# Kernel tuning notes

Hardware: AMD Instinct MI355X
Metric: run time of the kernel (lower is better)

## Reference

```python
import jax, jax.numpy as jnp
import numpy as np

N_QUBITS = 16
N_LAYERS = 6
BATCH = 512


def _apply_1q(state, U, q, n, batched):
    """Apply a single-qubit gate U to qubit q of state (B, 2**n).
    U: (2,2) shared, or (B,2,2) per-sample if batched."""
    B = state.shape[0]
    d0, d1 = 2 ** q, 2 ** (n - q - 1)
    s = state.reshape(B, d0, 2, d1)
    if batched:
        s = jnp.einsum('bij,bxjy->bxiy', U, s)
    else:
        s = jnp.einsum('ij,bxjy->bxiy', U, s)
    return s.reshape(B, -1)


def _apply_cnot(state, c, t, n):
    """CNOT with control c, target t on state (B, 2**n)."""
    B = state.shape[0]
    a, b = (c, t) if c < t else (t, c)
    d0, d1, d2 = 2 ** a, 2 ** (b - a - 1), 2 ** (n - b - 1)
    s = state.reshape(B, d0, 2, d1, 2, d2)
    if c < t:  # control = axis 2, target = axis 4: flip target where control==1
        s = jnp.concatenate([s[:, :, :1], jnp.flip(s[:, :, 1:], axis=4)], axis=2)
    else:      # control = axis 4, target = axis 2
        s = jnp.concatenate([s[:, :, :, :, :1], jnp.flip(s[:, :, :, :, 1:], axis=2)], axis=4)
    return s.reshape(B, -1)


def _rx(theta):
    """RX(theta) for a batch of angles -> (B,2,2) complex64."""
    c = jnp.cos(theta * 0.5).astype(jnp.complex64)
    s = (-1j * jnp.sin(theta * 0.5)).astype(jnp.complex64)
    return jnp.stack([jnp.stack([c, s], -1), jnp.stack([s, c], -1)], -2)


def _rot(phi, theta, omega):
    """PennyLane Rot(phi,theta,omega) = RZ(omega) RY(theta) RZ(phi) -> (2,2) complex64."""
    c = jnp.cos(theta * 0.5)
    s = jnp.sin(theta * 0.5)
    m00 = jnp.exp(-0.5j * (phi + omega)) * c
    m01 = -jnp.exp(0.5j * (phi - omega)) * s
    m10 = jnp.exp(-0.5j * (phi - omega)) * s
    m11 = jnp.exp(0.5j * (phi + omega)) * c
    return jnp.stack([jnp.stack([m00, m01]), jnp.stack([m10, m11])]).astype(jnp.complex64)


def _circuit(x, weights, n, n_layers):
    B = x.shape[0]
    state = jnp.zeros((B, 2 ** n), dtype=jnp.complex64).at[:, 0].set(1.0)
    # AngleEmbedding: default rotation is RX(x_q) on wire q (per-sample angles)
    for q in range(n):
        state = _apply_1q(state, _rx(x[:, q]), q, n, batched=True)
    # StronglyEntanglingLayers: Rot on each wire, then ring of CNOTs with range r
    for l in range(n_layers):
        for q in range(n):
            U = _rot(weights[l, q, 0], weights[l, q, 1], weights[l, q, 2])
            state = _apply_1q(state, U, q, n, batched=False)
        r = (l % (n - 1)) + 1  # PennyLane default ranges
        for q in range(n):
            state = _apply_cnot(state, q, (q + r) % n, n)
    # <Z_q> = P(bit_q = 0) - P(bit_q = 1)
    probs = state.real ** 2 + state.imag ** 2  # (B, 2**n)
    exps = []
    for q in range(n):
        p = probs.reshape(B, 2 ** q, 2, -1).sum(axis=(1, 3))  # (B, 2)
        exps.append(p[:, 0] - p[:, 1])
    return jnp.stack(exps, axis=-1)  # (B, n)


def setup_inputs() -> dict:
    key = jax.random.key(0)
    kx, kw = jax.random.split(key)
    x = jax.random.normal(kx, (BATCH, N_QUBITS), dtype=jnp.float32)
    weights = jax.random.normal(kw, (N_LAYERS, N_QUBITS, 3), dtype=jnp.float32)
    return {"x": x, "weights": weights}


def reference(x, weights):
    return _circuit(x, weights, N_QUBITS, N_LAYERS)
```

## Files before the change

kernel.cpp:

```cpp
#include <hip/hip_runtime.h>


#define NTH 512
typedef float v16f __attribute__((ext_vector_type(16)));

template <int I> struct IC { static constexpr int value = I; };
template <int N, int I = 0, typename F>
__device__ __forceinline__ void static_for(F&& f) {
  if constexpr (I < N) { f(IC<I>{}); static_for<N, I + 1>(f); }
}

template <int SH, int E> struct EIdx { static constexpr int v = (E & 1) | ((E >> 1) << SH); };


template <int LB>
__device__ __forceinline__ void rot_local(v16f& ar, v16f& ai, const float* __restrict__ u) {
  const float u00r = u[0], u00i = u[1], u01r = u[2], u01i = u[3];
  const float u10r = u[4], u10i = u[5], u11r = u[6], u11i = u[7];
  static_for<8>([&](auto hc) {
    constexpr int h = hc.value;
    constexpr int e0 = ((h >> LB) << (LB + 1)) | (h & ((1 << LB) - 1));
    constexpr int e1 = e0 | (1 << LB);
    const float axr = ar[e0], axi = ai[e0], bxr = ar[e1], bxi = ai[e1];
    ar[e0] = u00r * axr - u00i * axi + u01r * bxr - u01i * bxi;
    ai[e0] = u00r * axi + u00i * axr + u01r * bxi + u01i * bxr;
    ar[e1] = u10r * axr - u10i * axi + u11r * bxr - u11i * bxi;
    ai[e1] = u10r * axi + u10i * axr + u11r * bxi + u11i * bxr;
  });
}

__device__ __forceinline__ void rot_lane(v16f& ar, v16f& ai, const float* __restrict__ u,
                                         const int m, const int bit) {
  const float car = bit ? u[6] : u[0], cai = bit ? u[7] : u[1];
  const float cbr = bit ? u[4] : u[2], cbi = bit ? u[5] : u[3];
  static_for<16>([&](auto ec) {
    constexpr int e = ec.value;
    const float orr = ar[e], oii = ai[e];
    const float pr = __shfl_xor(orr, m);
    const float pi = __shfl_xor(oii, m);
    ar[e] = car * orr - cai * oii + cbr * pr - cbi * pi;
    ai[e] = car * oii + cai * orr + cbr * pi + cbi * pr;
  });
}

template <int SH, int C>
__device__ __forceinline__ void cnot_lane(v16f& ar, v16f& ai, const int m, const int ibase) {
  if constexpr ((EIdx<SH, 15>::v >> C) & 1) {
    static_for<16>([&](auto ec) {
      constexpr int e = ec.value;
      if constexpr ((EIdx<SH, e>::v >> C) & 1) {
        ar[e] = __shfl_xor(ar[e], m);
        ai[e] = __shfl_xor(ai[e], m);
      }
    });
  } else {
    if ((ibase >> C) & 1) {
      static_for<16>([&](auto ec) {
        constexpr int e = ec.value;
        ar[e] = __shfl_xor(ar[e], m);
        ai[e] = __shfl_xor(ai[e], m);
      });
    }
  }
}

template <int TB, int SH, int C>
__device__ __forceinline__ void cnot_local(v16f& ar, v16f& ai, const int ibase) {
  static_for<8>([&](auto hc) {
    constexpr int h = hc.value;
    constexpr int e0 = ((h >> TB) << (TB + 1)) | (h & ((1 << TB) - 1));
    constexpr int e1 = e0 | (1 << TB);
    if constexpr ((EIdx<SH, 15>::v >> C) & 1) {
      if constexpr ((EIdx<SH, e0>::v >> C) & 1) {
        const float tr = ar[e0], ti = ai[e0];
        ar[e0] = ar[e1]; ai[e0] = ai[e1];
        ar[e1] = tr;     ai[e1] = ti;
      }
    } else {
      const int take = (ibase >> C) & 1;
      const float axr = ar[e0], axi = ai[e0], bxr = ar[e1], bxi = ai[e1];
      ar[e0] = take ? bxr : axr; ai[e0] = take ? bxi : axi;
      ar[e1] = take ? axr : bxr; ai[e1] = take ? axi : bxi;
    }
  });
}

__global__ void qsim_prep(const float* __restrict__ w, float* __restrict__ gm) {
  const int i = threadIdx.x;
  if (i < 96) {
    const float phi = w[i * 3 + 0];
    const float th  = w[i * 3 + 1];
    const float om  = w[i * 3 + 2];
    float st, ct; sincosf(0.5f * th, &st, &ct);
    float sa, ca; sincosf(0.5f * (phi + om), &sa, &ca);
    float sb, cb; sincosf(0.5f * (phi - om), &sb, &cb);
    float* u = gm + i * 8;
    u[0] =  ct * ca; u[1] = -ct * sa;
    u[2] = -st * cb; u[3] = -st * sb;
    u[4] =  st * cb; u[5] = -st * sb;
    u[6] =  ct * ca; u[7] =  ct * sa;
  }
}

template <int L>
__global__ void __launch_bounds__(NTH) sweepP(float2* __restrict__ st,
                                              const float* __restrict__ x,
                                              const float* __restrict__ gm) {
  const int tid = threadIdx.x;
  const int s  = blockIdx.x >> 3;
  const int fb = blockIdx.x & 7;
  const int ibase = ((tid & 7) << 4) | (((tid >> 3) & 7) << 7) |
                    (((tid >> 6) & 7) << 10) | (fb << 13);
  const int pbase = ((tid & 7) << 1) | (((tid >> 6) & 7) << 7) | (fb << 10) |
                    (((tid >> 3) & 7) << 13);
  float2* __restrict__ base = st + (s << 16) + pbase;
  constexpr int r = L + 1;
  const float* __restrict__ gl = gm + L * 128;
  v16f ar, ai;

  if constexpr (L == 0) {
    __shared__ float iv[16][4];
    if (tid < 16) {
      const float* u = gm + tid * 8;
      float sx, cx; sincosf(0.5f * x[s * 16 + tid], &sx, &cx);
      iv[tid][0] = u[0] * cx + u[3] * sx;
      iv[tid][1] = u[1] * cx - u[2] * sx;
      iv[tid][2] = u[4] * cx + u[7] * sx;
      iv[tid][3] = u[5] * cx - u[6] * sx;
    }
    __syncthreads();
    float Tr = 1.f, Ti = 0.f;
    #pragma unroll
    for (int b = 4; b <= 15; ++b) {
      const int bit = (ibase >> b) & 1;
      const float fr = iv[b][2 * bit], fi = iv[b][2 * bit + 1];
      const float nr = Tr * fr - Ti * fi; Ti = Tr * fi + Ti * fr; Tr = nr;
    }
    ar[0] = Tr; ai[0] = Ti;
    static_for<4>([&](auto bc) {
      constexpr int bI = bc.value;
      const float v0r = iv[bI][0], v0i = iv[bI][1], v1r = iv[bI][2], v1i = iv[bI][3];
      static_for<(1 << bI)>([&](auto kc) {
        constexpr int k = kc.value;
        constexpr int k1 = k | (1 << bI);
        const float kr = ar[k], ki = ai[k];
        ar[k1] = kr * v1r - ki * v1i; ai[k1] = kr * v1i + ki * v1r;
        ar[k]  = kr * v0r - ki * v0i; ai[k]  = kr * v0i + ki * v0r;
      });
    });
  } else {
    #pragma unroll
    for (int eh = 0; eh < 8; ++eh) {
      const float4 v = *reinterpret_cast<const float4*>(base + (eh << 4));
      ar[2 * eh] = v.x; ai[2 * eh] = v.y; ar[2 * eh + 1] = v.z; ai[2 * eh + 1] = v.w;
    }
    static_for<L>([&](auto kc) {
      constexpr int k = kc.value;
      constexpr int C = 16 - L + k;
      if constexpr (k <= 3) cnot_local<k, 1, C>(ar, ai, ibase);
      else                  cnot_lane<1, C>(ar, ai, 1 << (k - 4), ibase);
    });
    rot_local<0>(ar, ai, gl);
    rot_local<1>(ar, ai, gl + 8);
    rot_local<2>(ar, ai, gl + 16);
    rot_local<3>(ar, ai, gl + 24);
    #pragma unroll
    for (int q = 4; q <= 9; ++q)
      rot_lane(ar, ai, gl + q * 8, 1 << (q - 4), (tid >> (q - 4)) & 1);
  }

  static_for<10 - r>([&](auto gc) {
    constexpr int g = gc.value;
    constexpr int t = g + r;
    if constexpr (t <= 3) cnot_local<t, 1, g>(ar, ai, ibase);
    else                  cnot_lane<1, g>(ar, ai, 1 << (t - 4), ibase);
  });

  #pragma unroll
  for (int eh = 0; eh < 8; ++eh)
    *reinterpret_cast<float4*>(base + (eh << 4)) =
        make_float4(ar[2 * eh], ai[2 * eh], ar[2 * eh + 1], ai[2 * eh + 1]);
}

template <int L>
__global__ void __launch_bounds__(NTH) sweepQ(float2* __restrict__ st,
                                              const float* __restrict__ gm) {
  const int tid = threadIdx.x;
  const int s  = blockIdx.x >> 3;
  const int fb = blockIdx.x & 7;
  const int ibase = ((tid & 7) << 4) | (((tid >> 3) & 7) << 13) |
                    (((tid >> 6) & 7) << 7) | (fb << 1);
  const int pbase = ((tid & 7) << 1) | (((tid >> 3) & 7) << 10) |
                    (((tid >> 6) & 7) << 13) | (fb << 4);
  float2* __restrict__ base = st + (s << 16) + pbase;
  constexpr int r = L + 1;
  const float* __restrict__ gl = gm + L * 128;
  v16f ar, ai;
  #pragma unroll
  for (int eh = 0; eh < 8; ++eh) {
    const float4 v = *reinterpret_cast<const float4*>(base + (eh << 7));
    ar[2 * eh] = v.x; ai[2 * eh] = v.y; ar[2 * eh + 1] = v.z; ai[2 * eh + 1] = v.w;
  }
  if constexpr (L > 0) {
    rot_local<1>(ar, ai, gl + 80);
    rot_local<2>(ar, ai, gl + 88);
    rot_local<3>(ar, ai, gl + 96);
    rot_lane(ar, ai, gl + 104, 8,  (tid >> 3) & 1);
    rot_lane(ar, ai, gl + 112, 16, (tid >> 4) & 1);
    rot_lane(ar, ai, gl + 120, 32, (tid >> 5) & 1);
  }
  static_for<6>([&](auto gc) {
    constexpr int g = 10 - r + gc.value;
    constexpr int t = g + r;
    if constexpr (t >= 13) cnot_lane<10, g>(ar, ai, 1 << (t - 10), ibase);
    else                   cnot_local<t - 9, 10, g>(ar, ai, ibase);
  });

  #pragma unroll
  for (int eh = 0; eh < 8; ++eh)
    *reinterpret_cast<float4*>(base + (eh << 7)) =
        make_float4(ar[2 * eh], ai[2 * eh], ar[2 * eh + 1], ai[2 * eh + 1]);
}

__global__ void __launch_bounds__(NTH) finalK(const float2* __restrict__ st,
                                              float* __restrict__ part) {
  const int tid = threadIdx.x;
  const int s  = blockIdx.x >> 3;
  const int fb = blockIdx.x & 7;
  const int ibase = ((tid & 7) << 4) | (((tid >> 3) & 7) << 7) |
                    (((tid >> 6) & 7) << 10) | (fb << 13);
  const int pbase = ((tid & 7) << 1) | (((tid >> 6) & 7) << 7) | (fb << 10) |
                    (((tid >> 3) & 7) << 13);
  const float2* __restrict__ base = st + (s << 16) + pbase;
  v16f ar, ai;
  #pragma unroll
  for (int eh = 0; eh < 8; ++eh) {
    const float4 v = *reinterpret_cast<const float4*>(base + (eh << 4));
    ar[2 * eh] = v.x; ai[2 * eh] = v.y; ar[2 * eh + 1] = v.z; ai[2 * eh + 1] = v.w;
  }
  static_for<6>([&](auto kc) {
    constexpr int k = kc.value;
    constexpr int C = 10 + k;
    if constexpr (k <= 3) cnot_local<k, 1, C>(ar, ai, ibase);
    else                  cnot_lane<1, C>(ar, ai, 1 << (k - 4), ibase);
  });
  __shared__ float red[8][16];
  float tot = 0.f, sl0 = 0.f, sl1 = 0.f, sl2 = 0.f, sl3 = 0.f;
  static_for<16>([&](auto ec) {
    constexpr int e = ec.value;
    const float p = ar[e] * ar[e] + ai[e] * ai[e];
    tot += p;
    if constexpr (e & 1) sl0 -= p; else sl0 += p;
    if constexpr (e & 2) sl1 -= p; else sl1 += p;
    if constexpr (e & 4) sl2 -= p; else sl2 += p;
    if constexpr (e & 8) sl3 -= p; else sl3 += p;
  });
  const float sl[4] = {sl0, sl1, sl2, sl3};
  const int wv = tid >> 6;
  static_for<16>([&](auto qc) {
    constexpr int q = qc.value;
    float v;
    if constexpr (q < 4) v = sl[q];
    else v = ((ibase >> q) & 1) ? -tot : tot;
    v += __shfl_xor(v, 1);  v += __shfl_xor(v, 2);  v += __shfl_xor(v, 4);
    v += __shfl_xor(v, 8);  v += __shfl_xor(v, 16); v += __shfl_xor(v, 32);
    if ((tid & 63) == 0) red[wv][q] = v;
  });
  __syncthreads();
  if (tid < 16) {
    float a = 0.f;
    #pragma unroll
    for (int w8 = 0; w8 < 8; ++w8) a += red[w8][tid];
    part[blockIdx.x * 16 + tid] = a;
  }
}

__global__ void __launch_bounds__(NTH) reduceK(const float* __restrict__ part,
                                               float* __restrict__ out) {
  const int j = blockIdx.x * NTH + threadIdx.x;
  const int s = j >> 4, q = j & 15;
  float a = 0.f;
  #pragma unroll
  for (int fb = 0; fb < 8; ++fb) a += part[(s << 7) + fb * 16 + q];
  out[j] = a;
}

extern "C" void kernel_launch(void* const* d_in, const int* in_sizes, int n_in,
                              void* d_out, int out_size, void* d_ws, size_t ws_size,
                              hipStream_t stream) {
  (void)in_sizes; (void)n_in; (void)out_size;
  const float* x = (const float*)d_in[0];
  const float* w = (const float*)d_in[1];
  float* out = (float*)d_out;
  float* gm   = (float*)d_ws;
  float* part = (float*)((char*)d_ws + 4096);
  float2* st  = (float2*)((char*)d_ws + 524288);

  const size_t avail = ws_size > 524288 ? ws_size - 524288 : 0;
  long long chunk = (long long)(avail / 524288);
  if (chunk > 256) chunk = 256;
  if (chunk < 1) chunk = 1;

  qsim_prep<<<dim3(1), dim3(128), 0, stream>>>(w, gm);
  for (int s0 = 0; s0 < 512; s0 += (int)chunk) {
    const int ns = (512 - s0) < (int)chunk ? (512 - s0) : (int)chunk;
    const dim3 g(ns * 8), b(NTH);
    const float* xs = x + s0 * 16;
    float* pp = part + (size_t)s0 * 128;
    sweepP<0><<<g, b, 0, stream>>>(st, xs, gm);
    sweepQ<0><<<g, b, 0, stream>>>(st, gm);
    sweepP<1><<<g, b, 0, stream>>>(st, xs, gm);
    sweepQ<1><<<g, b, 0, stream>>>(st, gm);
    sweepP<2><<<g, b, 0, stream>>>(st, xs, gm);
    sweepQ<2><<<g, b, 0, stream>>>(st, gm);
    sweepP<3><<<g, b, 0, stream>>>(st, xs, gm);
    sweepQ<3><<<g, b, 0, stream>>>(st, gm);
    sweepP<4><<<g, b, 0, stream>>>(st, xs, gm);
    sweepQ<4><<<g, b, 0, stream>>>(st, gm);
    sweepP<5><<<g, b, 0, stream>>>(st, xs, gm);
    sweepQ<5><<<g, b, 0, stream>>>(st, gm);
    finalK<<<g, b, 0, stream>>>(st, pp);
  }
  reduceK<<<dim3(16), dim3(NTH), 0, stream>>>(part, out);
}
```

Measured before the change: 1.579 ms.

## Move some rot_lane gates into the preceding kernel and use nontemporal stores

Some single-qubit rotations on lane-distributed qubits of the next layer are moved from the first sweep kernel into the end of the second sweep kernel, for the qubits whose CNOT dependencies allow it. This rebalances the per-kernel work and cuts the number of cross-lane shuffle gates in the first kernel. Global stores and the final load are switched to nontemporal builtins to reduce cache pollution on the streaming state. The risk is that reordering gates across kernels breaks correctness if the commutation assumptions are wrong, and nontemporal hints may bypass caches that were helping the reloads.

```diff
diff --git a/kernel.cpp b/kernel.cpp
--- a/kernel.cpp
+++ b/kernel.cpp
@@ -3,11 +3,20 @@
 
 #define NTH 512
 typedef float v16f __attribute__((ext_vector_type(16)));
+typedef float f4 __attribute__((ext_vector_type(4)));
 
 template <int I> struct IC { static constexpr int value = I; };
 template <int N, int I = 0, typename F>
 __device__ __forceinline__ void static_for(F&& f) {
   if constexpr (I < N) { f(IC<I>{}); static_for<N, I + 1>(f); }
+}
+
+__device__ __forceinline__ void nt_store4(float2* p, float a, float b, float c, float d) {
+  f4 v; v.x = a; v.y = b; v.z = c; v.w = d;
+  __builtin_nontemporal_store(v, reinterpret_cast<f4*>(p));
+}
+__device__ __forceinline__ f4 nt_load4(const float2* p) {
+  return __builtin_nontemporal_load(reinterpret_cast<const f4*>(p));
 }
 
 template <int SH, int E> struct EIdx { static constexpr int v = (E & 1) | ((E >> 1) << SH); };
@@ -164,9 +173,10 @@
     rot_local<1>(ar, ai, gl + 8);
     rot_local<2>(ar, ai, gl + 16);
     rot_local<3>(ar, ai, gl + 24);
-    #pragma unroll
-    for (int q = 4; q <= 9; ++q)
-      rot_lane(ar, ai, gl + q * 8, 1 << (q - 4), (tid >> (q - 4)) & 1);
+    if constexpr (L == 5) rot_lane(ar, ai, gl + 32, 1, tid & 1);
+    rot_lane(ar, ai, gl + 56, 8,  (tid >> 3) & 1);
+    rot_lane(ar, ai, gl + 64, 16, (tid >> 4) & 1);
+    rot_lane(ar, ai, gl + 72, 32, (tid >> 5) & 1);
   }
 
   static_for<10 - r>([&](auto gc) {
@@ -178,8 +188,7 @@
 
   #pragma unroll
   for (int eh = 0; eh < 8; ++eh)
-    *reinterpret_cast<float4*>(base + (eh << 4)) =
-        make_float4(ar[2 * eh], ai[2 * eh], ar[2 * eh + 1], ai[2 * eh + 1]);
+    nt_store4(base + (eh << 4), ar[2 * eh], ai[2 * eh], ar[2 * eh + 1], ai[2 * eh + 1]);
 }
 
 template <int L>
@@ -215,11 +224,21 @@
     if constexpr (t >= 13) cnot_lane<10, g>(ar, ai, 1 << (t - 10), ibase);
     else                   cnot_local<t - 9, 10, g>(ar, ai, ibase);
   });
+  if constexpr (L <= 3) {
+    const float* __restrict__ gn = gm + (L + 1) * 128;
+    rot_lane(ar, ai, gn + 32, 1, tid & 1);
+    rot_lane(ar, ai, gn + 40, 2, (tid >> 1) & 1);
+    rot_lane(ar, ai, gn + 48, 4, (tid >> 2) & 1);
+  }
+  if constexpr (L == 4) {
+    const float* __restrict__ gn = gm + 5 * 128;
+    rot_lane(ar, ai, gn + 40, 2, (tid >> 1) & 1);
+    rot_lane(ar, ai, gn + 48, 4, (tid >> 2) & 1);
+  }
 
   #pragma unroll
   for (int eh = 0; eh < 8; ++eh)
-    *reinterpret_cast<float4*>(base + (eh << 7)) =
-        make_float4(ar[2 * eh], ai[2 * eh], ar[2 * eh + 1], ai[2 * eh + 1]);
+    nt_store4(base + (eh << 7), ar[2 * eh], ai[2 * eh], ar[2 * eh + 1], ai[2 * eh + 1]);
 }
 
 __global__ void __launch_bounds__(NTH) finalK(const float2* __restrict__ st,
@@ -235,7 +254,7 @@
   v16f ar, ai;
   #pragma unroll
   for (int eh = 0; eh < 8; ++eh) {
-    const float4 v = *reinterpret_cast<const float4*>(base + (eh << 4));
+    const f4 v = nt_load4(base + (eh << 4));
     ar[2 * eh] = v.x; ai[2 * eh] = v.y; ar[2 * eh + 1] = v.z; ai[2 * eh + 1] = v.w;
   }
   static_for<6>([&](auto kc) {
```

Result: no change. 1.596 ms (+1.1%).

## Hold 32 amplitudes per thread and remap qubit bits across sweep kernels

Applied to the files above, without the earlier changes.

Doubles the per-thread register tile from 16 to 32 complex amplitudes, so each thread keeps 5 qubits local and blocks cover a quarter of a sample instead of an eighth. The qubit-to-register/lane/block bit mappings in sweepP, sweepQ and finalK are reworked so more gates and CNOTs run in registers and fewer need lane shuffles. The cnot and rot helpers are generalised to the new layout. The intent is less shuffle and grid overhead per gate, at the cost of higher register pressure and, in sweepQ, narrower strided float2 accesses instead of float4 loads.

```diff
diff --git a/kernel.cpp b/kernel.cpp
--- a/kernel.cpp
+++ b/kernel.cpp
@@ -2,7 +2,7 @@
 
 
 #define NTH 512
-typedef float v16f __attribute__((ext_vector_type(16)));
+typedef float v32f __attribute__((ext_vector_type(32)));
 
 template <int I> struct IC { static constexpr int value = I; };
 template <int N, int I = 0, typename F>
@@ -10,14 +10,12 @@
   if constexpr (I < N) { f(IC<I>{}); static_for<N, I + 1>(f); }
 }
 
-template <int SH, int E> struct EIdx { static constexpr int v = (E & 1) | ((E >> 1) << SH); };
-
 
 template <int LB>
-__device__ __forceinline__ void rot_local(v16f& ar, v16f& ai, const float* __restrict__ u) {
+__device__ __forceinline__ void rot_local(v32f& ar, v32f& ai, const float* __restrict__ u) {
   const float u00r = u[0], u00i = u[1], u01r = u[2], u01i = u[3];
   const float u10r = u[4], u10i = u[5], u11r = u[6], u11i = u[7];
-  static_for<8>([&](auto hc) {
+  static_for<16>([&](auto hc) {
     constexpr int h = hc.value;
     constexpr int e0 = ((h >> LB) << (LB + 1)) | (h & ((1 << LB) - 1));
     constexpr int e1 = e0 | (1 << LB);
@@ -29,11 +27,11 @@
   });
 }
 
-__device__ __forceinline__ void rot_lane(v16f& ar, v16f& ai, const float* __restrict__ u,
+__device__ __forceinline__ void rot_lane(v32f& ar, v32f& ai, const float* __restrict__ u,
                                          const int m, const int bit) {
   const float car = bit ? u[6] : u[0], cai = bit ? u[7] : u[1];
   const float cbr = bit ? u[4] : u[2], cbi = bit ? u[5] : u[3];
-  static_for<16>([&](auto ec) {
+  static_for<32>([&](auto ec) {
     constexpr int e = ec.value;
     const float orr = ar[e], oii = ai[e];
     const float pr = __shfl_xor(orr, m);
@@ -43,35 +41,14 @@
   });
 }
 
-template <int SH, int C>
-__device__ __forceinline__ void cnot_lane(v16f& ar, v16f& ai, const int m, const int ibase) {
-  if constexpr ((EIdx<SH, 15>::v >> C) & 1) {
-    static_for<16>([&](auto ec) {
-      constexpr int e = ec.value;
-      if constexpr ((EIdx<SH, e>::v >> C) & 1) {
-        ar[e] = __shfl_xor(ar[e], m);
-        ai[e] = __shfl_xor(ai[e], m);
-      }
-    });
-  } else {
-    if ((ibase >> C) & 1) {
-      static_for<16>([&](auto ec) {
-        constexpr int e = ec.value;
-        ar[e] = __shfl_xor(ar[e], m);
-        ai[e] = __shfl_xor(ai[e], m);
-      });
-    }
-  }
-}
-
-template <int TB, int SH, int C>
-__device__ __forceinline__ void cnot_local(v16f& ar, v16f& ai, const int ibase) {
-  static_for<8>([&](auto hc) {
+template <int TB, int LOCALLO, int C>
+__device__ __forceinline__ void cnot_local(v32f& ar, v32f& ai, const int ibase) {
+  static_for<16>([&](auto hc) {
     constexpr int h = hc.value;
     constexpr int e0 = ((h >> TB) << (TB + 1)) | (h & ((1 << TB) - 1));
     constexpr int e1 = e0 | (1 << TB);
-    if constexpr ((EIdx<SH, 15>::v >> C) & 1) {
-      if constexpr ((EIdx<SH, e0>::v >> C) & 1) {
+    if constexpr (C >= LOCALLO && C < LOCALLO + 5) {
+      if constexpr ((e0 >> (C - LOCALLO)) & 1) {
         const float tr = ar[e0], ti = ai[e0];
         ar[e0] = ar[e1]; ai[e0] = ai[e1];
         ar[e1] = tr;     ai[e1] = ti;
@@ -83,6 +60,28 @@
       ar[e1] = take ? axr : bxr; ai[e1] = take ? axi : bxi;
     }
   });
+}
+
+template <int LOCALLO, int C>
+__device__ __forceinline__ void cnot_lane(v32f& ar, v32f& ai, const int m, const int ibase) {
+  if constexpr (C >= LOCALLO && C < LOCALLO + 5) {
+    static_for<32>([&](auto ec) {
+      constexpr int e = ec.value;
+      if constexpr ((e >> (C - LOCALLO)) & 1) {
+        ar[e] = __shfl_xor(ar[e], m);
+        ai[e] = __shfl_xor(ai[e], m);
+      }
+    });
+  } else {
+    const int take = (ibase >> C) & 1;
+    static_for<32>([&](auto ec) {
+      constexpr int e = ec.value;
+      const float pr = __shfl_xor(ar[e], m);
+      const float pi = __shfl_xor(ai[e], m);
+      ar[e] = take ? pr : ar[e];
+      ai[e] = take ? pi : ai[e];
+    });
+  }
 }
 
 __global__ void qsim_prep(const float* __restrict__ w, float* __restrict__ gm) {
@@ -107,16 +106,16 @@
                                               const float* __restrict__ x,
                                               const float* __restrict__ gm) {
   const int tid = threadIdx.x;
-  const int s  = blockIdx.x >> 3;
-  const int fb = blockIdx.x & 7;
-  const int ibase = ((tid & 7) << 4) | (((tid >> 3) & 7) << 7) |
-                    (((tid >> 6) & 7) << 10) | (fb << 13);
-  const int pbase = ((tid & 7) << 1) | (((tid >> 6) & 7) << 7) | (fb << 10) |
-                    (((tid >> 3) & 7) << 13);
+  const int s  = blockIdx.x >> 2;
+  const int fb = blockIdx.x & 3;
+  const int ibase = (((tid >> 3) & 7) << 5) | (((tid >> 6) & 7) << 8) |
+                    (fb << 11) | ((tid & 7) << 13);
+  const int pbase = (((tid >> 3) & 7) << 1) | ((tid & 7) << 4) |
+                    (((tid >> 6) & 7) << 11) | (fb << 14);
   float2* __restrict__ base = st + (s << 16) + pbase;
   constexpr int r = L + 1;
   const float* __restrict__ gl = gm + L * 128;
-  v16f ar, ai;
+  v32f ar, ai;
 
   if constexpr (L == 0) {
     __shared__ float iv[16][4];
@@ -131,13 +130,13 @@
     __syncthreads();
     float Tr = 1.f, Ti = 0.f;
     #pragma unroll
-    for (int b = 4; b <= 15; ++b) {
+    for (int b = 5; b <= 15; ++b) {
       const int bit = (ibase >> b) & 1;
       const float fr = iv[b][2 * bit], fi = iv[b][2 * bit + 1];
       const float nr = Tr * fr - Ti * fi; Ti = Tr * fi + Ti * fr; Tr = nr;
     }
     ar[0] = Tr; ai[0] = Ti;
-    static_for<4>([&](auto bc) {
+    static_for<5>([&](auto bc) {
       constexpr int bI = bc.value;
       const float v0r = iv[bI][0], v0i = iv[bI][1], v1r = iv[bI][2], v1i = iv[bI][3];
       static_for<(1 << bI)>([&](auto kc) {
@@ -150,35 +149,36 @@
     });
   } else {
     #pragma unroll
-    for (int eh = 0; eh < 8; ++eh) {
-      const float4 v = *reinterpret_cast<const float4*>(base + (eh << 4));
+    for (int eh = 0; eh < 16; ++eh) {
+      const float4 v = *reinterpret_cast<const float4*>(base + (eh << 7));
       ar[2 * eh] = v.x; ai[2 * eh] = v.y; ar[2 * eh + 1] = v.z; ai[2 * eh + 1] = v.w;
     }
     static_for<L>([&](auto kc) {
       constexpr int k = kc.value;
       constexpr int C = 16 - L + k;
-      if constexpr (k <= 3) cnot_local<k, 1, C>(ar, ai, ibase);
-      else                  cnot_lane<1, C>(ar, ai, 1 << (k - 4), ibase);
+      if constexpr (k <= 4) cnot_local<k, 0, C>(ar, ai, ibase);
+      else                  cnot_lane<0, C>(ar, ai, 8, ibase);
     });
     rot_local<0>(ar, ai, gl);
     rot_local<1>(ar, ai, gl + 8);
     rot_local<2>(ar, ai, gl + 16);
     rot_local<3>(ar, ai, gl + 24);
-    #pragma unroll
-    for (int q = 4; q <= 9; ++q)
-      rot_lane(ar, ai, gl + q * 8, 1 << (q - 4), (tid >> (q - 4)) & 1);
-  }
-
-  static_for<10 - r>([&](auto gc) {
+    rot_local<4>(ar, ai, gl + 32);
+    rot_lane(ar, ai, gl + 40, 8,  (tid >> 3) & 1);
+    rot_lane(ar, ai, gl + 48, 16, (tid >> 4) & 1);
+    rot_lane(ar, ai, gl + 56, 32, (tid >> 5) & 1);
+  }
+
+  static_for<8 - r>([&](auto gc) {
     constexpr int g = gc.value;
     constexpr int t = g + r;
-    if constexpr (t <= 3) cnot_local<t, 1, g>(ar, ai, ibase);
-    else                  cnot_lane<1, g>(ar, ai, 1 << (t - 4), ibase);
-  });
-
-  #pragma unroll
-  for (int eh = 0; eh < 8; ++eh)
-    *reinterpret_cast<float4*>(base + (eh << 4)) =
+    if constexpr (t <= 4) cnot_local<t, 0, g>(ar, ai, ibase);
+    else                  cnot_lane<0, g>(ar, ai, 1 << (t - 2), ibase);
+  });
+
+  #pragma unroll
+  for (int eh = 0; eh < 16; ++eh)
+    *reinterpret_cast<float4*>(base + (eh << 7)) =
         make_float4(ar[2 * eh], ai[2 * eh], ar[2 * eh + 1], ai[2 * eh + 1]);
 }
 
@@ -186,81 +186,86 @@
 __global__ void __launch_bounds__(NTH) sweepQ(float2* __restrict__ st,
                                               const float* __restrict__ gm) {
   const int tid = threadIdx.x;
-  const int s  = blockIdx.x >> 3;
-  const int fb = blockIdx.x & 7;
-  const int ibase = ((tid & 7) << 4) | (((tid >> 3) & 7) << 13) |
-                    (((tid >> 6) & 7) << 7) | (fb << 1);
-  const int pbase = ((tid & 7) << 1) | (((tid >> 3) & 7) << 10) |
-                    (((tid >> 6) & 7) << 13) | (fb << 4);
+  const int s  = blockIdx.x >> 2;
+  const int fb = blockIdx.x & 3;
+  const int ibase = ((tid >> 6) & 7) | (fb << 3) | ((tid & 7) << 5) |
+                    (((tid >> 3) & 7) << 13);
+  const int pbase = ((tid >> 6) & 1) | ((tid & 7) << 1) | (((tid >> 3) & 7) << 4) |
+                    (((tid >> 7) & 1) << 7) | (((tid >> 8) & 1) << 8) |
+                    ((fb & 1) << 9) | (((fb >> 1) & 1) << 10);
   float2* __restrict__ base = st + (s << 16) + pbase;
   constexpr int r = L + 1;
   const float* __restrict__ gl = gm + L * 128;
-  v16f ar, ai;
-  #pragma unroll
-  for (int eh = 0; eh < 8; ++eh) {
-    const float4 v = *reinterpret_cast<const float4*>(base + (eh << 7));
-    ar[2 * eh] = v.x; ai[2 * eh] = v.y; ar[2 * eh + 1] = v.z; ai[2 * eh + 1] = v.w;
+  v32f ar, ai;
+  #pragma unroll
+  for (int e = 0; e < 32; ++e) {
+    const float2 v = base[e << 11];
+    ar[e] = v.x; ai[e] = v.y;
   }
   if constexpr (L > 0) {
-    rot_local<1>(ar, ai, gl + 80);
-    rot_local<2>(ar, ai, gl + 88);
-    rot_local<3>(ar, ai, gl + 96);
+    rot_local<0>(ar, ai, gl + 64);
+    rot_local<1>(ar, ai, gl + 72);
+    rot_local<2>(ar, ai, gl + 80);
+    rot_local<3>(ar, ai, gl + 88);
+    rot_local<4>(ar, ai, gl + 96);
     rot_lane(ar, ai, gl + 104, 8,  (tid >> 3) & 1);
     rot_lane(ar, ai, gl + 112, 16, (tid >> 4) & 1);
     rot_lane(ar, ai, gl + 120, 32, (tid >> 5) & 1);
   }
-  static_for<6>([&](auto gc) {
-    constexpr int g = 10 - r + gc.value;
+  static_for<8>([&](auto gc) {
+    constexpr int g = 8 - r + gc.value;
     constexpr int t = g + r;
-    if constexpr (t >= 13) cnot_lane<10, g>(ar, ai, 1 << (t - 10), ibase);
-    else                   cnot_local<t - 9, 10, g>(ar, ai, ibase);
-  });
-
-  #pragma unroll
-  for (int eh = 0; eh < 8; ++eh)
-    *reinterpret_cast<float4*>(base + (eh << 7)) =
-        make_float4(ar[2 * eh], ai[2 * eh], ar[2 * eh + 1], ai[2 * eh + 1]);
+    if constexpr (t <= 12) cnot_local<t - 8, 8, g>(ar, ai, ibase);
+    else                   cnot_lane<8, g>(ar, ai, 1 << (t - 10), ibase);
+  });
+
+  #pragma unroll
+  for (int e = 0; e < 32; ++e) {
+    float2 v; v.x = ar[e]; v.y = ai[e];
+    base[e << 11] = v;
+  }
 }
 
 __global__ void __launch_bounds__(NTH) finalK(const float2* __restrict__ st,
                                               float* __restrict__ part) {
   const int tid = threadIdx.x;
-  const int s  = blockIdx.x >> 3;
-  const int fb = blockIdx.x & 7;
-  const int ibase = ((tid & 7) << 4) | (((tid >> 3) & 7) << 7) |
-                    (((tid >> 6) & 7) << 10) | (fb << 13);
-  const int pbase = ((tid & 7) << 1) | (((tid >> 6) & 7) << 7) | (fb << 10) |
-                    (((tid >> 3) & 7) << 13);
+  const int s  = blockIdx.x >> 2;
+  const int fb = blockIdx.x & 3;
+  const int ibase = (((tid >> 3) & 7) << 5) | (((tid >> 6) & 7) << 8) |
+                    (fb << 11) | ((tid & 7) << 13);
+  const int pbase = (((tid >> 3) & 7) << 1) | ((tid & 7) << 4) |
+                    (((tid >> 6) & 7) << 11) | (fb << 14);
   const float2* __restrict__ base = st + (s << 16) + pbase;
-  v16f ar, ai;
-  #pragma unroll
-  for (int eh = 0; eh < 8; ++eh) {
-    const float4 v = *reinterpret_cast<const float4*>(base + (eh << 4));
+  v32f ar, ai;
+  #pragma unroll
+  for (int eh = 0; eh < 16; ++eh) {
+    const float4 v = *reinterpret_cast<const float4*>(base + (eh << 7));
     ar[2 * eh] = v.x; ai[2 * eh] = v.y; ar[2 * eh + 1] = v.z; ai[2 * eh + 1] = v.w;
   }
   static_for<6>([&](auto kc) {
     constexpr int k = kc.value;
     constexpr int C = 10 + k;
-    if constexpr (k <= 3) cnot_local<k, 1, C>(ar, ai, ibase);
-    else                  cnot_lane<1, C>(ar, ai, 1 << (k - 4), ibase);
+    if constexpr (k <= 4) cnot_local<k, 0, C>(ar, ai, ibase);
+    else                  cnot_lane<0, C>(ar, ai, 8, ibase);
   });
   __shared__ float red[8][16];
-  float tot = 0.f, sl0 = 0.f, sl1 = 0.f, sl2 = 0.f, sl3 = 0.f;
-  static_for<16>([&](auto ec) {
+  float tot = 0.f, sl0 = 0.f, sl1 = 0.f, sl2 = 0.f, sl3 = 0.f, sl4 = 0.f;
+  static_for<32>([&](auto ec) {
     constexpr int e = ec.value;
     const float p = ar[e] * ar[e] + ai[e] * ai[e];
     tot += p;
-    if constexpr (e & 1) sl0 -= p; else sl0 += p;
-    if constexpr (e & 2) sl1 -= p; else sl1 += p;
-    if constexpr (e & 4) sl2 -= p; else sl2 += p;
-    if constexpr (e & 8) sl3 -= p; else sl3 += p;
-  });
-  const float sl[4] = {sl0, sl1, sl2, sl3};
+    if constexpr (e & 1)  sl0 -= p; else sl0 += p;
+    if constexpr (e & 2)  sl1 -= p; else sl1 += p;
+    if constexpr (e & 4)  sl2 -= p; else sl2 += p;
+    if constexpr (e & 8)  sl3 -= p; else sl3 += p;
+    if constexpr (e & 16) sl4 -= p; else sl4 += p;
+  });
+  const float sl[5] = {sl0, sl1, sl2, sl3, sl4};
   const int wv = tid >> 6;
   static_for<16>([&](auto qc) {
     constexpr int q = qc.value;
     float v;
-    if constexpr (q < 4) v = sl[q];
+    if constexpr (q < 5) v = sl[q];
     else v = ((ibase >> q) & 1) ? -tot : tot;
     v += __shfl_xor(v, 1);  v += __shfl_xor(v, 2);  v += __shfl_xor(v, 4);
     v += __shfl_xor(v, 8);  v += __shfl_xor(v, 16); v += __shfl_xor(v, 32);
@@ -281,7 +286,7 @@
   const int s = j >> 4, q = j & 15;
   float a = 0.f;
   #pragma unroll
-  for (int fb = 0; fb < 8; ++fb) a += part[(s << 7) + fb * 16 + q];
+  for (int f = 0; f < 4; ++f) a += part[(s << 6) + f * 16 + q];
   out[j] = a;
 }
 
@@ -304,9 +309,9 @@
   qsim_prep<<<dim3(1), dim3(128), 0, stream>>>(w, gm);
   for (int s0 = 0; s0 < 512; s0 += (int)chunk) {
     const int ns = (512 - s0) < (int)chunk ? (512 - s0) : (int)chunk;
-    const dim3 g(ns * 8), b(NTH);
+    const dim3 g(ns * 4), b(NTH);
     const float* xs = x + s0 * 16;
-    float* pp = part + (size_t)s0 * 128;
+    float* pp = part + (size_t)s0 * 64;
     sweepP<0><<<g, b, 0, stream>>>(st, xs, gm);
     sweepQ<0><<<g, b, 0, stream>>>(st, gm);
     sweepP<1><<<g, b, 0, stream>>>(st, xs, gm);
```

Measured after the change: 1.770 ms. 1.12x slower.
